# Performance work log

Hardware: AMD Instinct MI355X
Metric: run time of the kernel (lower is better)

Reference implementation:

```python
import jax, jax.numpy as jnp
import numpy as np

B, N, H, C = 8, 128, 768, 5


def setup_inputs() -> dict:
    key = jax.random.key(0)
    k0, k1, k2, k3 = jax.random.split(key, 4)
    h = jax.random.normal(k0, (B, N, H), dtype=jnp.float32)
    # torch nn.Linear(4H, H): out = x @ W.T + b; we store Wcat = W.T with shape [4H, H]
    Wcat = jax.random.normal(k1, (4 * H, H), dtype=jnp.float32) * 0.02
    bW = jnp.zeros((H,), dtype=jnp.float32)
    h_hat = jax.random.normal(k2, (H,), dtype=jnp.float32)
    Wout = jax.random.normal(k3, (H, C), dtype=jnp.float32) * 0.02
    bout = jnp.zeros((C,), dtype=jnp.float32)
    return {"h": h, "Wcat": Wcat, "bW": bW, "h_hat": h_hat, "Wout": Wout, "bout": bout}


def reference(h, Wcat, bW, h_hat, Wout, bout):
    n = h.shape[1]
    W1, W2, W3, W4 = jnp.split(Wcat, 4, axis=0)  # each [H, H]
    # span order matches the torch double loop: i in range(N), j in range(i, N)
    ii, jj = jnp.triu_indices(n)  # P = n(n+1)/2
    # cat([hi,hj,hi-hj,hi*hj]) @ Wcat == hi@(W1+W3) + hj@(W2-W3) + (hi*hj)@W4
    A = jnp.einsum('bnh,hk->bnk', h, W1 + W3)   # [B, N, H]
    Bm = jnp.einsum('bnh,hk->bnk', h, W2 - W3)  # [B, N, H]
    prod = h[:, ii, :] * h[:, jj, :]            # [B, P, H]
    spans = jnp.tanh(A[:, ii, :] + Bm[:, jj, :]
                     + jnp.einsum('bph,hk->bpk', prod, W4) + bW)  # [B, P, H]
    # InterpretationLayer: attention pooling over spans
    alpha = jax.nn.softmax(jnp.einsum('bph,h->bp', spans, h_hat), axis=1)
    h_tilde = jnp.einsum('bp,bph->bh', alpha, spans)  # [B, H]
    logits = h_tilde @ Wout + bout                    # [B, C]
    return jax.nn.log_softmax(logits, axis=1)
```

## Files before the change

### kernel.cpp

```cpp
#include <hip/hip_runtime.h>
#include <hip/hip_bf16.h>


#define B_ 8
#define N_ 128
#define H_ 768
#define C_ 5
#define P_ 8256
#define TP 96
#define NBLK 86
#define NSTEP 24
#define SLABK 128
#define NSLAB 6

typedef short bf16x8 __attribute__((ext_vector_type(8)));
typedef float f32x4 __attribute__((ext_vector_type(4)));

__device__ __forceinline__ float bf2f(unsigned short u){
  union { unsigned u; float f; } v; v.u = ((unsigned)u) << 16; return v.f;
}
__device__ __forceinline__ unsigned short f2bf(float f){
  union { float f; unsigned u; } v; v.f = f;
  unsigned r = v.u + 0x7FFFu + ((v.u >> 16) & 1u);
  return (unsigned short)(r >> 16);
}
__device__ __forceinline__ float tanh_fast(float x){
  float e = __expf(2.f * x);
  return 1.f - 2.f / (e + 1.f);
}
__device__ __forceinline__ bf16x8 prodpack(bf16x8 x, bf16x8 y){
  union { bf16x8 v; unsigned u[4]; } o;
  #pragma unroll
  for (int e2 = 0; e2 < 4; e2++){
    float p0 = bf2f((unsigned short)x[e2*2])   * bf2f((unsigned short)y[e2*2]);
    float p1 = bf2f((unsigned short)x[e2*2+1]) * bf2f((unsigned short)y[e2*2+1]);
    unsigned pk;
    asm volatile("v_cvt_pk_bf16_f32 %0, %1, %2" : "=v"(pk) : "v"(p0), "v"(p1));
    o.u[e2] = pk;
  }
  return o.v;
}
__device__ __forceinline__ int lds_off(int row, int k){
  return row * (H_ * 2) + ((k * 2) ^ ((row & 15) << 4));
}


#define PH_BLKS 3072
#define PW_BLKS 288
#define PR_BLKS 33

__global__ void prep(const float* __restrict__ h, const float* __restrict__ Wcat,
                     unsigned short* __restrict__ hb,
                     unsigned short* __restrict__ Wsum,
                     unsigned short* __restrict__ Wdif,
                     unsigned short* __restrict__ W4s,
                     int* __restrict__ ii, int* __restrict__ jj){
  const int bid = blockIdx.x;
  if (bid < PH_BLKS){
    int idx = bid * 256 + threadIdx.x;
    hb[idx] = f2bf(h[idx]);
  } else if (bid < PH_BLKS + PW_BLKS){
    int idx = (bid - PH_BLKS) * 256 + threadIdx.x;
    int o = idx / H_, col = idx % H_;
    bf16x8 vs, vd, v4;
    #pragma unroll
    for (int e = 0; e < 8; e++){
      int hrow = o * 8 + e;
      float w1 = Wcat[hrow * H_ + col];
      float w2 = Wcat[(H_ + hrow) * H_ + col];
      float w3 = Wcat[(2 * H_ + hrow) * H_ + col];
      float w4 = Wcat[(3 * H_ + hrow) * H_ + col];
      vs[e] = (short)f2bf(w1 + w3);
      vd[e] = (short)f2bf(w2 - w3);
      v4[e] = (short)f2bf(w4);
    }
    int pbase = (o * H_ + col) * 8;
    *(bf16x8*)(Wsum + pbase) = vs;
    *(bf16x8*)(Wdif + pbase) = vd;
    *(bf16x8*)(W4s + pbase)  = v4;
  } else {
    int p = (bid - PH_BLKS - PW_BLKS) * 256 + threadIdx.x;
    if (p < P_){
      int i = 0, off = 0;
      while (off + (N_ - i) <= p){ off += (N_ - i); i++; }
      ii[p] = i; jj[p] = i + (p - off);
    }
  }
}


__global__ __launch_bounds__(512, 4) void coef_gemm(
    const unsigned short* __restrict__ hb,
    const unsigned short* __restrict__ Wsum,
    const unsigned short* __restrict__ Wdif,
    const float* __restrict__ bW,
    float* __restrict__ Acoef, float* __restrict__ Bcoef){
  const int sel = blockIdx.y;
  const unsigned short* Wp = sel ? Wdif : Wsum;
  float* out = sel ? Bcoef : Acoef;
  const int growb = blockIdx.x * 16;

  __shared__ char As[16 * H_ * 2];

  const int tid = threadIdx.x;
  {
    int r = tid >> 5;
    int c = tid & 31;
    const unsigned short* src = hb + (growb + r) * H_;
    #pragma unroll
    for (int kk = 0; kk < 3; kk++){
      int k = kk * 256 + c * 8;
      bf16x8 v = *(const bf16x8*)(src + k);
      *(bf16x8*)(As + lds_off(r, k)) = v;
    }
  }
  __syncthreads();

  const int lane = tid & 63;
  const int wn = tid >> 6;
  const int hi = lane >> 4;
  const int l15 = lane & 15;
  const int colbase = wn * 96 + l15;

  f32x4 acc[6] = {};

  const bf16x8* wp = (const bf16x8*)Wp + hi * H_ + colbase;
  bf16x8 bc0 = wp[0], bc1 = wp[16], bc2 = wp[32], bc3 = wp[48], bc4 = wp[64], bc5 = wp[80];
  wp += 4 * H_;
  for (int step = 0; step < 24; ++step){
    bf16x8 bn0 = wp[0], bn1 = wp[16], bn2 = wp[32], bn3 = wp[48], bn4 = wp[64], bn5 = wp[80];
    wp += 4 * H_;
    bf16x8 a = *(const bf16x8*)(As + lds_off(l15, step * 32 + hi * 8));
    acc[0] = __builtin_amdgcn_mfma_f32_16x16x32_bf16(a, bc0, acc[0], 0, 0, 0);
    acc[1] = __builtin_amdgcn_mfma_f32_16x16x32_bf16(a, bc1, acc[1], 0, 0, 0);
    acc[2] = __builtin_amdgcn_mfma_f32_16x16x32_bf16(a, bc2, acc[2], 0, 0, 0);
    acc[3] = __builtin_amdgcn_mfma_f32_16x16x32_bf16(a, bc3, acc[3], 0, 0, 0);
    acc[4] = __builtin_amdgcn_mfma_f32_16x16x32_bf16(a, bc4, acc[4], 0, 0, 0);
    acc[5] = __builtin_amdgcn_mfma_f32_16x16x32_bf16(a, bc5, acc[5], 0, 0, 0);
    bc0 = bn0; bc1 = bn1; bc2 = bn2; bc3 = bn3; bc4 = bn4; bc5 = bn5;
  }

  #pragma unroll
  for (int ni = 0; ni < 6; ni++){
    int col = colbase + ni * 16;
    float bw = (sel == 0) ? bW[col] : 0.f;
    #pragma unroll
    for (int r = 0; r < 4; r++){
      int grow = growb + hi * 4 + r;
      out[grow * H_ + col] = acc[ni][r] + bw;
    }
  }
}


#define STEP_BODY(T, BCUR, BNXT)                                             \
  {                                                                          \
    if ((T) + 1 < NSTEP){                                                    \
      _Pragma("unroll")                                                      \
      for (int ni = 0; ni < 6; ni++)                                         \
        BNXT[ni] = wp[(((T) + 1) * 4 + hi) * H_ + colbase + ni * 16];        \
    }                                                                        \
    const int klb = ((T) & 3) * 64 + hi * 16;                                \
    bf16x8 a[6];                                                             \
    _Pragma("unroll")                                                        \
    for (int mg = 0; mg < 6; mg++)                                           \
      a[mg] = *(const bf16x8*)(pcur + (mg * 16 + l15) * 256 + (klb ^ (l15 << 4))); \
    __builtin_amdgcn_s_setprio(1);                                           \
    _Pragma("unroll")                                                        \
    for (int ni = 0; ni < 6; ni++){                                          \
      _Pragma("unroll")                                                      \
      for (int mg = 0; mg < 6; mg++)                                         \
        acc[mg][ni] = __builtin_amdgcn_mfma_f32_16x16x32_bf16(a[mg], BCUR[ni], acc[mg][ni], 0, 0, 0); \
    }                                                                        \
    __builtin_amdgcn_s_setprio(0);                                           \
  }

__global__ __launch_bounds__(512, 2)
void spans_fused(
    const unsigned short* __restrict__ hb,
    const float* __restrict__ Acoef,
    const float* __restrict__ Bcoef,
    const unsigned short* __restrict__ W4s,
    const float* __restrict__ hhat,
    const int* __restrict__ ii,
    const int* __restrict__ jj,
    float* __restrict__ pm, float* __restrict__ pl, float* __restrict__ pacc){
  __shared__ char Pp[2][TP * 256];
  __shared__ int iis[TP], jjs[TP];
  __shared__ float sbuf[8][TP];
  __shared__ float wbuf[TP];
  __shared__ float Msh;

  const int bid = blockIdx.x;
  const int b = bid / NBLK;
  const int p0 = (bid % NBLK) * TP;
  const int tid = threadIdx.x;

  if (tid < TP){ iis[tid] = ii[p0 + tid]; jjs[tid] = jj[p0 + tid]; }
  __syncthreads();

  const int lane = tid & 63;
  const int wave = tid >> 6;
  const int hi = lane >> 4;
  const int l15 = lane & 15;
  const int colbase = wave * 96 + l15;

  int rch[3], cch[3];
  const unsigned short *hpr[3], *hqr[3];
  #pragma unroll
  for (int t = 0; t < 3; t++){
    int cid = tid + t * 512;
    rch[t] = cid >> 4; cch[t] = cid & 15;
    hpr[t] = hb + (b * N_ + iis[rch[t]]) * H_;
    hqr[t] = hb + (b * N_ + jjs[rch[t]]) * H_;
  }

  bf16x8 va[3], vb[3];
  #pragma unroll
  for (int t = 0; t < 3; t++){
    va[t] = *(const bf16x8*)(hpr[t] + cch[t] * 8);
    vb[t] = *(const bf16x8*)(hqr[t] + cch[t] * 8);
  }

  f32x4 acc[6][6];
  #pragma unroll
  for (int mg = 0; mg < 6; mg++){
    #pragma unroll
    for (int r = 0; r < 4; r++){
      int rowl = mg * 16 + hi * 4 + r;
      const float* ap = Acoef + (b * N_ + iis[rowl]) * H_ + colbase;
      const float* bp = Bcoef + (b * N_ + jjs[rowl]) * H_ + colbase;
      #pragma unroll
      for (int ni = 0; ni < 6; ni++)
        acc[mg][ni][r] = ap[ni * 16] + bp[ni * 16];
    }
  }

  #pragma unroll
  for (int t = 0; t < 3; t++)
    *(bf16x8*)(Pp[0] + rch[t] * 256 + ((cch[t] * 16) ^ ((rch[t] & 15) << 4))) =
        prodpack(va[t], vb[t]);

  const bf16x8* wp = (const bf16x8*)W4s;
  bf16x8 bA[6], bB[6];
  #pragma unroll
  for (int ni = 0; ni < 6; ni++)
    bA[ni] = wp[hi * H_ + colbase + ni * 16];

  __syncthreads();

  for (int slab = 0; slab < NSLAB; ++slab){
    const char* pcur = Pp[slab & 1];
    if (slab + 1 < NSLAB){
      const int kg = (slab + 1) * SLABK;
      #pragma unroll
      for (int t = 0; t < 3; t++){
        va[t] = *(const bf16x8*)(hpr[t] + kg + cch[t] * 8);
        vb[t] = *(const bf16x8*)(hqr[t] + kg + cch[t] * 8);
      }
    }
    const int t0 = slab * 4;
    STEP_BODY(t0,     bA, bB);
    STEP_BODY(t0 + 1, bB, bA);
    STEP_BODY(t0 + 2, bA, bB);
    STEP_BODY(t0 + 3, bB, bA);
    if (slab + 1 < NSLAB){
      #pragma unroll
      for (int t = 0; t < 3; t++)
        *(bf16x8*)(Pp[(slab & 1) ^ 1] + rch[t] * 256 +
                   ((cch[t] * 16) ^ ((rch[t] & 15) << 4))) = prodpack(va[t], vb[t]);
    }
    __syncthreads();
  }

  float sc[6][4];
  #pragma unroll
  for (int mg = 0; mg < 6; mg++)
    #pragma unroll
    for (int r = 0; r < 4; r++) sc[mg][r] = 0.f;

  #pragma unroll
  for (int ni = 0; ni < 6; ni++){
    float hh = hhat[colbase + ni * 16];
    #pragma unroll
    for (int mg = 0; mg < 6; mg++){
      #pragma unroll
      for (int r = 0; r < 4; r++){
        float s = tanh_fast(acc[mg][ni][r]);
        acc[mg][ni][r] = s;
        sc[mg][r] += s * hh;
      }
    }
  }
  #pragma unroll
  for (int mg = 0; mg < 6; mg++)
    #pragma unroll
    for (int r = 0; r < 4; r++){
      float v = sc[mg][r];
      v += __shfl_xor(v, 1); v += __shfl_xor(v, 2);
      v += __shfl_xor(v, 4); v += __shfl_xor(v, 8);
      sc[mg][r] = v;
    }
  if (l15 == 0){
    #pragma unroll
    for (int mg = 0; mg < 6; mg++)
      #pragma unroll
      for (int r = 0; r < 4; r++)
        sbuf[wave][mg * 16 + hi * 4 + r] = sc[mg][r];
  }
  __syncthreads();

  if (tid < TP){
    float s = 0.f;
    #pragma unroll
    for (int w = 0; w < 8; w++) s += sbuf[w][tid];
    wbuf[tid] = s;
  }
  __syncthreads();
  if (tid < 64){
    float a = wbuf[tid];
    float bq = (tid < 32) ? wbuf[64 + tid] : -3.4e38f;
    float m = fmaxf(a, bq);
    #pragma unroll
    for (int off = 1; off < 64; off <<= 1) m = fmaxf(m, __shfl_xor(m, off));
    float l = __expf(a - m) + ((tid < 32) ? __expf(bq - m) : 0.f);
    #pragma unroll
    for (int off = 1; off < 64; off <<= 1) l += __shfl_xor(l, off);
    if (tid == 0){ pm[bid] = m; pl[bid] = l; Msh = m; }
  }
  __syncthreads();
  if (tid < TP) wbuf[tid] = __expf(wbuf[tid] - Msh);
  __syncthreads();

  #pragma unroll
  for (int ni = 0; ni < 6; ni++){
    float wa = 0.f;
    #pragma unroll
    for (int mg = 0; mg < 6; mg++)
      #pragma unroll
      for (int r = 0; r < 4; r++)
        wa += wbuf[mg * 16 + hi * 4 + r] * acc[mg][ni][r];
    wa += __shfl_xor(wa, 16);
    wa += __shfl_xor(wa, 32);
    if (lane < 16) pacc[bid * H_ + colbase + ni * 16] = wa;
  }
}


__global__ void merge1(
    const float* __restrict__ pm, const float* __restrict__ pl,
    const float* __restrict__ pacc, float* __restrict__ htg){
  __shared__ float ebuf[NBLK];
  __shared__ float Msh, invLsh;
  __shared__ float part[128];
  const int b = blockIdx.x;
  const int ch = blockIdx.y;
  const int tid = threadIdx.x;

  if (tid < 64){
    float m = -3.4e38f;
    for (int t = tid; t < NBLK; t += 64) m = fmaxf(m, pm[b * NBLK + t]);
    #pragma unroll
    for (int off = 1; off < 64; off <<= 1) m = fmaxf(m, __shfl_xor(m, off));
    float l = 0.f;
    for (int t = tid; t < NBLK; t += 64) l += pl[b * NBLK + t] * __expf(pm[b * NBLK + t] - m);
    #pragma unroll
    for (int off = 1; off < 64; off <<= 1) l += __shfl_xor(l, off);
    if (tid == 0){ Msh = m; invLsh = 1.f / l; }
  }
  __syncthreads();
  if (tid < NBLK) ebuf[tid] = __expf(pm[b * NBLK + tid] - Msh);
  __syncthreads();
  const int col = ch * 128 + (tid & 127);
  const int half = tid >> 7;
  float a = 0.f;
  for (int t = half; t < NBLK; t += 2) a += pacc[(b * NBLK + t) * H_ + col] * ebuf[t];
  if (half) part[tid & 127] = a;
  __syncthreads();
  if (!half) htg[b * H_ + col] = (a + part[tid]) * invLsh;
}


__global__ void merge2(
    const float* __restrict__ htg,
    const float* __restrict__ Wout, const float* __restrict__ bout,
    float* __restrict__ outp){
  const int b = blockIdx.x;
  const int lane = threadIdx.x;
  float a[C_] = {};
  for (int k = lane; k < H_; k += 64){
    float hv = htg[b * H_ + k];
    #pragma unroll
    for (int c = 0; c < C_; c++) a[c] += hv * Wout[k * C_ + c];
  }
  #pragma unroll
  for (int c = 0; c < C_; c++){
    #pragma unroll
    for (int off = 1; off < 64; off <<= 1) a[c] += __shfl_xor(a[c], off);
  }
  if (lane == 0){
    float lg[C_];
    #pragma unroll
    for (int c = 0; c < C_; c++) lg[c] = a[c] + bout[c];
    float mx = lg[0];
    #pragma unroll
    for (int c = 1; c < C_; c++) mx = fmaxf(mx, lg[c]);
    float s = 0.f;
    #pragma unroll
    for (int c = 0; c < C_; c++) s += __expf(lg[c] - mx);
    float ls = __logf(s) + mx;
    #pragma unroll
    for (int c = 0; c < C_; c++) outp[b * C_ + c] = lg[c] - ls;
  }
}


extern "C" void kernel_launch(void* const* d_in, const int* in_sizes, int n_in,
                              void* d_out, int out_size, void* d_ws, size_t ws_size,
                              hipStream_t stream){
  const float* h    = (const float*)d_in[0];
  const float* Wcat = (const float*)d_in[1];
  const float* bW   = (const float*)d_in[2];
  const float* hhat = (const float*)d_in[3];
  const float* Wout = (const float*)d_in[4];
  const float* bout = (const float*)d_in[5];
  float* outp = (float*)d_out;

  unsigned short* hb   = (unsigned short*)d_ws;
  unsigned short* Wsum = hb + 786432;
  unsigned short* Wdif = Wsum + 589824;
  unsigned short* W4s  = Wdif + 589824;
  float* Acoef = (float*)(W4s + 589824);
  float* Bcoef = Acoef + 786432;
  int* iiA = (int*)(Bcoef + 786432);
  int* jjA = iiA + P_;
  float* pm = (float*)(jjA + P_);
  float* pl = pm + (B_ * NBLK);
  float* pacc = pl + (B_ * NBLK);
  float* htg  = pacc + (B_ * NBLK * H_);

  prep<<<PH_BLKS + PW_BLKS + PR_BLKS, 256, 0, stream>>>(h, Wcat, hb, Wsum, Wdif, W4s, iiA, jjA);
  coef_gemm<<<dim3(64, 2), 512, 0, stream>>>(hb, Wsum, Wdif, bW, Acoef, Bcoef);
  spans_fused<<<B_ * NBLK, 512, 0, stream>>>(hb, Acoef, Bcoef, W4s, hhat, iiA, jjA, pm, pl, pacc);
  merge1<<<dim3(B_, 6), 256, 0, stream>>>(pm, pl, pacc, htg);
  merge2<<<B_, 64, 0, stream>>>(htg, Wout, bout, outp);
}
```

Before: 188.9 us.

## Stage W4 slabs in LDS via async global_load_lds and store coefficients as bf16

Each K-step's W4 slab is now loaded into a double-buffered LDS region with global_load_lds direct-to-LDS copies shared by all waves, replacing the per-wave register prefetch of W4 from global memory. The MFMA loop is restructured so it synchronises after every K-step rather than once per slab. The A/B coefficient tensors are also stored as bf16 instead of fp32, halving the gather traffic in the span kernel at some cost in precision. The extra barriers and the 96KB of added LDS may lower occupancy.

```diff
diff --git a/kernel.cpp b/kernel.cpp
--- a/kernel.cpp
+++ b/kernel.cpp
@@ -10,8 +10,7 @@
 #define TP 96
 #define NBLK 86
 #define NSTEP 24
-#define SLABK 128
-#define NSLAB 6
+#define BSLAB 49152
 
 typedef short bf16x8 __attribute__((ext_vector_type(8)));
 typedef float f32x4 __attribute__((ext_vector_type(4)));
@@ -39,6 +38,12 @@
     o.u[e2] = pk;
   }
   return o.v;
+}
+__device__ __forceinline__ void gload_lds16(const char* g, char* l){
+  __builtin_amdgcn_global_load_lds(
+      (const __attribute__((address_space(1))) unsigned int*)g,
+      (__attribute__((address_space(3))) unsigned int*)l,
+      16, 0, 0);
 }
 __device__ __forceinline__ int lds_off(int row, int k){
   return row * (H_ * 2) + ((k * 2) ^ ((row & 15) << 4));
@@ -94,10 +99,10 @@
     const unsigned short* __restrict__ Wsum,
     const unsigned short* __restrict__ Wdif,
     const float* __restrict__ bW,
-    float* __restrict__ Acoef, float* __restrict__ Bcoef){
+    unsigned short* __restrict__ Acoef, unsigned short* __restrict__ Bcoef){
   const int sel = blockIdx.y;
   const unsigned short* Wp = sel ? Wdif : Wsum;
-  float* out = sel ? Bcoef : Acoef;
+  unsigned short* out = sel ? Bcoef : Acoef;
   const int growb = blockIdx.x * 16;
 
   __shared__ char As[16 * H_ * 2];
@@ -147,44 +152,23 @@
     #pragma unroll
     for (int r = 0; r < 4; r++){
       int grow = growb + hi * 4 + r;
-      out[grow * H_ + col] = acc[ni][r] + bw;
-    }
-  }
-}
-
-
-#define STEP_BODY(T, BCUR, BNXT)                                             \
-  {                                                                          \
-    if ((T) + 1 < NSTEP){                                                    \
-      _Pragma("unroll")                                                      \
-      for (int ni = 0; ni < 6; ni++)                                         \
-        BNXT[ni] = wp[(((T) + 1) * 4 + hi) * H_ + colbase + ni * 16];        \
-    }                                                                        \
-    const int klb = ((T) & 3) * 64 + hi * 16;                                \
-    bf16x8 a[6];                                                             \
-    _Pragma("unroll")                                                        \
-    for (int mg = 0; mg < 6; mg++)                                           \
-      a[mg] = *(const bf16x8*)(pcur + (mg * 16 + l15) * 256 + (klb ^ (l15 << 4))); \
-    __builtin_amdgcn_s_setprio(1);                                           \
-    _Pragma("unroll")                                                        \
-    for (int ni = 0; ni < 6; ni++){                                          \
-      _Pragma("unroll")                                                      \
-      for (int mg = 0; mg < 6; mg++)                                         \
-        acc[mg][ni] = __builtin_amdgcn_mfma_f32_16x16x32_bf16(a[mg], BCUR[ni], acc[mg][ni], 0, 0, 0); \
-    }                                                                        \
-    __builtin_amdgcn_s_setprio(0);                                           \
-  }
+      out[grow * H_ + col] = f2bf(acc[ni][r] + bw);
+    }
+  }
+}
+
 
 __global__ __launch_bounds__(512, 2)
 void spans_fused(
     const unsigned short* __restrict__ hb,
-    const float* __restrict__ Acoef,
-    const float* __restrict__ Bcoef,
+    const unsigned short* __restrict__ Acoef,
+    const unsigned short* __restrict__ Bcoef,
     const unsigned short* __restrict__ W4s,
     const float* __restrict__ hhat,
     const int* __restrict__ ii,
     const int* __restrict__ jj,
     float* __restrict__ pm, float* __restrict__ pl, float* __restrict__ pacc){
+  __shared__ char Bsl[2][BSLAB];
   __shared__ char Pp[2][TP * 256];
   __shared__ int iis[TP], jjs[TP];
   __shared__ float sbuf[8][TP];
@@ -204,6 +188,8 @@
   const int hi = lane >> 4;
   const int l15 = lane & 15;
   const int colbase = wave * 96 + l15;
+  const char* w4b = (const char*)W4s;
+  const int bchunk = wave * 6144;
 
   int rch[3], cch[3];
   const unsigned short *hpr[3], *hqr[3];
@@ -221,6 +207,9 @@
     va[t] = *(const bf16x8*)(hpr[t] + cch[t] * 8);
     vb[t] = *(const bf16x8*)(hqr[t] + cch[t] * 8);
   }
+  #pragma unroll
+  for (int q = 0; q < 6; q++)
+    gload_lds16(w4b + bchunk + q * 1024 + lane * 16, Bsl[0] + bchunk + q * 1024);
 
   f32x4 acc[6][6];
   #pragma unroll
@@ -228,49 +217,63 @@
     #pragma unroll
     for (int r = 0; r < 4; r++){
       int rowl = mg * 16 + hi * 4 + r;
-      const float* ap = Acoef + (b * N_ + iis[rowl]) * H_ + colbase;
-      const float* bp = Bcoef + (b * N_ + jjs[rowl]) * H_ + colbase;
+      const unsigned short* ap = Acoef + (b * N_ + iis[rowl]) * H_ + colbase;
+      const unsigned short* bp = Bcoef + (b * N_ + jjs[rowl]) * H_ + colbase;
       #pragma unroll
       for (int ni = 0; ni < 6; ni++)
-        acc[mg][ni][r] = ap[ni * 16] + bp[ni * 16];
-    }
-  }
-
+        acc[mg][ni][r] = bf2f(ap[ni * 16]) + bf2f(bp[ni * 16]);
+    }
+  }
   #pragma unroll
   for (int t = 0; t < 3; t++)
     *(bf16x8*)(Pp[0] + rch[t] * 256 + ((cch[t] * 16) ^ ((rch[t] & 15) << 4))) =
         prodpack(va[t], vb[t]);
-
-  const bf16x8* wp = (const bf16x8*)W4s;
-  bf16x8 bA[6], bB[6];
-  #pragma unroll
-  for (int ni = 0; ni < 6; ni++)
-    bA[ni] = wp[hi * H_ + colbase + ni * 16];
-
-  __syncthreads();
-
-  for (int slab = 0; slab < NSLAB; ++slab){
-    const char* pcur = Pp[slab & 1];
-    if (slab + 1 < NSLAB){
-      const int kg = (slab + 1) * SLABK;
+  __syncthreads();
+
+  char* pcur = Pp[0];
+  char* pnxt = Pp[1];
+  for (int s = 0; s < 6; ++s){
+    if (s < 5){
+      const int kg = (s + 1) * 128;
       #pragma unroll
       for (int t = 0; t < 3; t++){
         va[t] = *(const bf16x8*)(hpr[t] + kg + cch[t] * 8);
         vb[t] = *(const bf16x8*)(hqr[t] + kg + cch[t] * 8);
       }
     }
-    const int t0 = slab * 4;
-    STEP_BODY(t0,     bA, bB);
-    STEP_BODY(t0 + 1, bB, bA);
-    STEP_BODY(t0 + 2, bA, bB);
-    STEP_BODY(t0 + 3, bB, bA);
-    if (slab + 1 < NSLAB){
-      #pragma unroll
-      for (int t = 0; t < 3; t++)
-        *(bf16x8*)(Pp[(slab & 1) ^ 1] + rch[t] * 256 +
-                   ((cch[t] * 16) ^ ((rch[t] & 15) << 4))) = prodpack(va[t], vb[t]);
-    }
-    __syncthreads();
+    #pragma unroll
+    for (int ts = 0; ts < 4; ++ts){
+      if (ts < 3 || s < 5){
+        const char* src = w4b + (s * 4 + ts + 1) * BSLAB + bchunk;
+        #pragma unroll
+        for (int q = 0; q < 6; q++)
+          gload_lds16(src + q * 1024 + lane * 16,
+                      Bsl[(ts + 1) & 1] + bchunk + q * 1024);
+      }
+      const char* bb = Bsl[ts & 1] + (hi * H_ + colbase) * 16;
+      bf16x8 bfr[6];
+      #pragma unroll
+      for (int ni = 0; ni < 6; ni++)
+        bfr[ni] = *(const bf16x8*)(bb + ni * 256);
+      const int klb = ts * 64 + hi * 16;
+      __builtin_amdgcn_s_setprio(1);
+      #pragma unroll
+      for (int mg = 0; mg < 6; mg++){
+        bf16x8 am = *(const bf16x8*)(pcur + (mg * 16 + l15) * 256 + (klb ^ (l15 << 4)));
+        #pragma unroll
+        for (int ni = 0; ni < 6; ni++)
+          acc[mg][ni] = __builtin_amdgcn_mfma_f32_16x16x32_bf16(am, bfr[ni], acc[mg][ni], 0, 0, 0);
+      }
+      __builtin_amdgcn_s_setprio(0);
+      if (ts == 3 && s < 5){
+        #pragma unroll
+        for (int t = 0; t < 3; t++)
+          *(bf16x8*)(pnxt + rch[t] * 256 + ((cch[t] * 16) ^ ((rch[t] & 15) << 4))) =
+              prodpack(va[t], vb[t]);
+      }
+      __syncthreads();
+    }
+    char* tmp = pcur; pcur = pnxt; pnxt = tmp;
   }
 
   float sc[6][4];
@@ -430,8 +433,8 @@
   unsigned short* Wsum = hb + 786432;
   unsigned short* Wdif = Wsum + 589824;
   unsigned short* W4s  = Wdif + 589824;
-  float* Acoef = (float*)(W4s + 589824);
-  float* Bcoef = Acoef + 786432;
+  unsigned short* Acoef = W4s + 589824;
+  unsigned short* Bcoef = Acoef + 786432;
   int* iiA = (int*)(Bcoef + 786432);
   int* jjA = iiA + P_;
   float* pm = (float*)(jjA + P_);
```

After: 283.8 us. 50.2% more time.
